# Optimization experiments

Hardware: AMD Instinct MI355X
Metric: run time of the kernel (lower is better)

Reference implementation:

```python
import jax, jax.numpy as jnp
import numpy as np

NUM_HEADS = 16
EMB = 1024
HEAD = 64
SEQ = 2048
BATCH = 4


def setup_inputs() -> dict:
    key = jax.random.key(0)
    ks = jax.random.split(key, 6)
    s = EMB ** -0.5
    x = jax.random.normal(ks[0], (BATCH, SEQ, EMB), dtype=jnp.float32)
    # per-head projection weights stacked: [H, E, D] (Linear(emb, head, bias=False) per head)
    Wq = jax.random.normal(ks[1], (NUM_HEADS, EMB, HEAD), dtype=jnp.float32) * s
    Wk = jax.random.normal(ks[2], (NUM_HEADS, EMB, HEAD), dtype=jnp.float32) * s
    Wv = jax.random.normal(ks[3], (NUM_HEADS, EMB, HEAD), dtype=jnp.float32) * s
    # output projection Linear(head*num_heads, emb): weight [E, H*D], bias [E]
    Wo = jax.random.normal(ks[4], (EMB, NUM_HEADS * HEAD), dtype=jnp.float32) * ((NUM_HEADS * HEAD) ** -0.5)
    bo = jax.random.normal(ks[5], (EMB,), dtype=jnp.float32) * 0.01
    return {"x": x, "Wq": Wq, "Wk": Wk, "Wv": Wv, "Wo": Wo, "bo": bo}


def reference(x, Wq, Wk, Wv, Wo, bo):
    B, S, E = x.shape
    scale = HEAD ** -0.5
    # batched per-head projections: [B, H, S, D]
    q = jnp.einsum('bse,hed->bhsd', x, Wq)
    k = jnp.einsum('bse,hed->bhsd', x, Wk)
    v = jnp.einsum('bse,hed->bhsd', x, Wv)
    scores = jnp.einsum('bhqd,bhkd->bhqk', q, k) * scale
    causal = jnp.tril(jnp.ones((S, S), dtype=bool))
    scores = jnp.where(causal, scores, jnp.finfo(scores.dtype).min)
    attn = jax.nn.softmax(scores, axis=-1)  # dropout disabled (eval/deterministic)
    ctx = jnp.einsum('bhqk,bhkd->bhqd', attn, v)
    # concat heads along last dim (head-major order, matching torch.cat)
    concat = ctx.transpose(0, 2, 1, 3).reshape(B, S, NUM_HEADS * HEAD)
    out = concat @ Wo.T + bo
    return out
```

## Files before the change

kernel.cpp:

```cpp
#include <hip/hip_runtime.h>

#define NHEADS 16
#define EMB 1024
#define HDIM 64
#define SEQ 2048
#define BATCH 4

typedef unsigned short u16;
typedef __attribute__((ext_vector_type(8))) __bf16 bf16x8;
typedef __attribute__((ext_vector_type(4))) float f32x4;

#if __has_builtin(__builtin_amdgcn_exp2f)
#define EXP2(x) __builtin_amdgcn_exp2f(x)
#else
#define EXP2(x) __expf((x)*0.69314718056f)
#endif
#define CL2E 0.18033688011112042f

#define BARRIER() __builtin_amdgcn_s_barrier()
#define SB0() __builtin_amdgcn_sched_barrier(0)
#define PRIO1() __builtin_amdgcn_s_setprio(1)
#define PRIO0() __builtin_amdgcn_s_setprio(0)
#define VMCNT(n) asm volatile("s_waitcnt vmcnt(" #n ")" ::: "memory")
#define LGKM0() asm volatile("s_waitcnt lgkmcnt(0)" ::: "memory")

__device__ __forceinline__ u16 f2bf(float f) {
  union { float f; unsigned u; } v; v.f = f;
  unsigned r = v.u + 0x7fffu + ((v.u >> 16) & 1u);
  return (u16)(r >> 16);
}
__device__ __forceinline__ unsigned pk2bf(float a, float b) {
  union { __bf16 h[2]; unsigned u; } x;
  x.h[0] = (__bf16)a; x.h[1] = (__bf16)b; return x.u;
}
__device__ __forceinline__ void gl16(const void* g, void* l) {
  __builtin_amdgcn_global_load_lds(
      (const __attribute__((address_space(1))) unsigned*)g,
      (__attribute__((address_space(3))) unsigned*)l, 16, 0, 0);
}
__device__ __forceinline__ unsigned PKLO(unsigned a, unsigned b) {
  return __builtin_amdgcn_perm(a, b, 0x01000504u);
}
__device__ __forceinline__ unsigned PKHI(unsigned a, unsigned b) {
  return __builtin_amdgcn_perm(a, b, 0x03020706u);
}

__global__ __launch_bounds__(256) void k_cvt(const float* __restrict__ in,
                                             u16* __restrict__ out, int n4) {
  int i = blockIdx.x * 256 + threadIdx.x;
  if (i >= n4) return;
  f32x4 v = *(const f32x4*)(in + (size_t)i * 4);
  uint2 o;
  o.x = (unsigned)f2bf(v[0]) | ((unsigned)f2bf(v[1]) << 16);
  o.y = (unsigned)f2bf(v[2]) | ((unsigned)f2bf(v[3]) << 16);
  *(uint2*)(out + (size_t)i * 4) = o;
}

__global__ __launch_bounds__(256) void k_packw(const float* __restrict__ Wq,
                                               const float* __restrict__ Wk,
                                               const float* __restrict__ Wv,
                                               u16* __restrict__ Wt) {
  const int mh = blockIdx.x;
  const int e0 = blockIdx.y * 64;
  const int mtx = mh >> 4, h = mh & 15;
  const float* W = (mtx == 0 ? Wq : (mtx == 1 ? Wk : Wv)) + (size_t)h * EMB * HDIM;
  __shared__ u16 sT[64][65];
  const int t = threadIdx.x;
  {
    int e = t >> 2, d0 = (t & 3) * 16;
#pragma unroll
    for (int jj = 0; jj < 4; jj++) {
      f32x4 v = *(const f32x4*)(W + (size_t)(e0 + e) * HDIM + d0 + jj * 4);
#pragma unroll
      for (int kk = 0; kk < 4; kk++) sT[e][d0 + jj * 4 + kk] = f2bf(v[kk]);
    }
  }
  __syncthreads();
  {
    int d = t >> 2, eb = (t & 3) * 16;
#pragma unroll
    for (int j = 0; j < 16; j++)
      Wt[(size_t)(mh * 64 + d) * EMB + e0 + eb + j] = sT[eb + j][d];
  }
}

__global__ __launch_bounds__(512, 2) void k_gemm_qkv8(const u16* __restrict__ Xb,
                                                      const u16* __restrict__ Wt,
                                                      u16* __restrict__ Q,
                                                      u16* __restrict__ K,
                                                      u16* __restrict__ V) {
  extern __shared__ __align__(16) char smem[];
  const int bid = blockIdx.x;
  const int l = (bid & 7) * 64 + (bid >> 3);
  const int mt = l & 31, nt = l >> 5;
  const int m0 = mt * 256, n0 = nt * 192;

  const int t = threadIdx.x;
  const int wave = t >> 6, lane = t & 63, lr = lane & 15, lg = lane >> 4;
  const int wr = (wave >> 2) * 128;
  const int wc = (wave & 3) * 48;

  const f32x4 fz = {0.f, 0.f, 0.f, 0.f};
  f32x4 acc[8][3];
#pragma unroll
  for (int i = 0; i < 8; i++)
#pragma unroll
    for (int j = 0; j < 3; j++) acc[i][j] = fz;

  bf16x8 af[4][2], bfr[3][2];

  auto SROUND = [&](char* ldsbase, int rbase, const u16* src, int gRowBase, int kt) {
    int rs = rbase + wave * 8;
    int row = rs + (lane >> 3);
    int gc = (lane & 7) ^ (row & 7);
    gl16(src + (size_t)(gRowBase + row) * EMB + kt * 64 + gc * 8, ldsbase + rs * 128);
  };
  auto LOADA = [&](const char* bA, int mh) {
#pragma unroll
    for (int mf = 0; mf < 4; mf++)
#pragma unroll
      for (int kf = 0; kf < 2; kf++) {
        int row = wr + mh * 64 + mf * 16 + lr;
        af[mf][kf] = *(const bf16x8*)(bA + row * 128 + ((kf * 64 + lg * 16) ^ ((row & 7) << 4)));
      }
  };
  auto LOADB = [&](const char* bB) {
#pragma unroll
    for (int nf = 0; nf < 3; nf++)
#pragma unroll
      for (int kf = 0; kf < 2; kf++) {
        int row = wc + nf * 16 + lr;
        bfr[nf][kf] = *(const bf16x8*)(bB + row * 128 + ((kf * 64 + lg * 16) ^ ((row & 7) << 4)));
      }
  };

#define MFMAPH(MH)                                                                         \
  do {                                                                                     \
    _Pragma("unroll") for (int kf = 0; kf < 2; kf++)                                       \
    _Pragma("unroll") for (int mf = 0; mf < 4; mf++)                                       \
    _Pragma("unroll") for (int nf = 0; nf < 3; nf++)                                       \
      acc[(MH)*4 + mf][nf] = __builtin_amdgcn_mfma_f32_16x16x32_bf16(                      \
          af[mf][kf], bfr[nf][kf], acc[(MH)*4 + mf][nf], 0, 0, 0);                         \
  } while (0)

  const int NT = EMB / 64;
  {
    char* nA = smem;
    char* nB = smem + 32768;
    SROUND(nB, 0, Wt, n0, 0); SROUND(nB, 64, Wt, n0, 0); SROUND(nB, 128, Wt, n0, 0);
    SROUND(nA, 0, Xb, m0, 0);
    SROUND(nA, 64, Xb, m0, 0); SROUND(nA, 128, Xb, m0, 0); SROUND(nA, 192, Xb, m0, 0);
  }
  VMCNT(0);
  BARRIER();

  for (int tt = 0; tt < NT - 1; tt++) {
    const int cb = tt & 1, nb = cb ^ 1;
    char* bA = smem + cb * 57344;
    char* bB = bA + 32768;
    char* nA = smem + nb * 57344;
    char* nB = nA + 32768;
    SROUND(nB, 0, Wt, n0, tt + 1);
    SROUND(nB, 64, Wt, n0, tt + 1);
    SROUND(nB, 128, Wt, n0, tt + 1);
    SROUND(nA, 0, Xb, m0, tt + 1);
    VMCNT(5);
    BARRIER(); SB0();
    LOADA(bA, 0);
    LOADB(bB);
    PRIO1(); MFMAPH(0); PRIO0();
    BARRIER();
    SROUND(nA, 64, Xb, m0, tt + 1);
    SROUND(nA, 128, Xb, m0, tt + 1);
    SROUND(nA, 192, Xb, m0, tt + 1);
    VMCNT(7);
    BARRIER(); SB0();
    LOADA(bA, 1);
    PRIO1(); MFMAPH(1); PRIO0();
    BARRIER();
  }
  {
    char* bA = smem + ((NT - 1) & 1) * 57344;
    char* bB = bA + 32768;
    VMCNT(0);
    BARRIER(); SB0();
    LOADA(bA, 0);
    LOADB(bB);
    PRIO1(); MFMAPH(0); PRIO0();
    LOADA(bA, 1);
    PRIO1(); MFMAPH(1); PRIO0();
  }
#undef MFMAPH

  const int b = m0 >> 11;
  const int s0 = m0 & 2047;
#pragma unroll
  for (int am = 0; am < 8; am++)
#pragma unroll
    for (int nf = 0; nf < 3; nf++)
#pragma unroll
      for (int r = 0; r < 4; r++) {
        int row = wr + am * 16 + lg * 4 + r;
        int n = n0 + wc + nf * 16 + lr;
        int mtx = n >> 10, h = (n >> 6) & 15, d = n & 63;
        u16* dst = (mtx == 0 ? Q : (mtx == 1 ? K : V));
        dst[((size_t)(b * NHEADS + h) * SEQ + s0 + row) * HDIM + d] = f2bf(acc[am][nf][r]);
      }
}

__global__ __launch_bounds__(256, 3) void k_attn(const u16* __restrict__ Q,
                                                 const u16* __restrict__ K,
                                                 const u16* __restrict__ V,
                                                 u16* __restrict__ Cc) {
  const int bh = blockIdx.x;
  const int qt = 15 - (int)blockIdx.y;
  const int b = bh >> 4, h = bh & 15;
  const int t = threadIdx.x;
  const int wq = t >> 6, lane = t & 63, lr = lane & 15, lg = lane >> 4;
  const size_t base = (size_t)bh * SEQ * HDIM;

  __shared__ __align__(16) char sK[2][64 * 128];
  __shared__ __align__(16) char sV[2][64 * 128];
  __shared__ __align__(16) char sP[128 * 128];

  const int kvb = (t & 15) * 4, db = (t >> 4) * 4;
  uint2 v0, v1, v2, v3;
  auto VLOAD = [&](int k0) {
    const u16* vp = V + base + (size_t)(k0 + kvb) * HDIM + db;
    v0 = *(const uint2*)(vp);
    v1 = *(const uint2*)(vp + HDIM);
    v2 = *(const uint2*)(vp + 2 * HDIM);
    v3 = *(const uint2*)(vp + 3 * HDIM);
  };
  auto VWRITE = [&](char* sv) {
    uint2 w0 = {PKLO(v0.x, v1.x), PKLO(v2.x, v3.x)};
    uint2 w1 = {PKHI(v0.x, v1.x), PKHI(v2.x, v3.x)};
    uint2 w2 = {PKLO(v0.y, v1.y), PKLO(v2.y, v3.y)};
    uint2 w3 = {PKHI(v0.y, v1.y), PKHI(v2.y, v3.y)};
    *(uint2*)(sv + (db + 0) * 128 + ((kvb * 2) ^ (((db + 0) & 7) << 4))) = w0;
    *(uint2*)(sv + (db + 1) * 128 + ((kvb * 2) ^ (((db + 1) & 7) << 4))) = w1;
    *(uint2*)(sv + (db + 2) * 128 + ((kvb * 2) ^ (((db + 2) & 7) << 4))) = w2;
    *(uint2*)(sv + (db + 3) * 128 + ((kvb * 2) ^ (((db + 3) & 7) << 4))) = w3;
  };
  auto KSTAGE = [&](char* sk, int k0) {
#pragma unroll
    for (int i = 0; i < 2; i++) {
      int rb = wq * 16 + i * 8;
      int row = rb + (lane >> 3);
      int gc = (lane & 7) ^ (row & 7);
      gl16(K + base + (size_t)(k0 + row) * HDIM + gc * 8, sk + rb * 128);
    }
  };

#pragma unroll
  for (int i = 0; i < 4; i++) {
    int rb = wq * 32 + i * 8;
    int row = rb + (lane >> 3);
    int gc = (lane & 7) ^ (row & 7);
    gl16(Q + base + (size_t)(qt * 128 + row) * HDIM + gc * 8, sP + rb * 128);
  }
  KSTAGE(sK[0], 0);
  VLOAD(0);
  VMCNT(0);
  VWRITE(sV[0]);
  __syncthreads();

  bf16x8 qf[2][2];
#pragma unroll
  for (int q2 = 0; q2 < 2; q2++)
#pragma unroll
    for (int kf = 0; kf < 2; kf++) {
      int row = wq * 32 + q2 * 16 + lr;
      qf[q2][kf] = *(const bf16x8*)(sP + row * 128 + ((kf * 64 + lg * 16) ^ ((row & 7) << 4)));
    }

  const f32x4 fz = {0.f, 0.f, 0.f, 0.f};
  f32x4 ot[4][2];
#pragma unroll
  for (int df = 0; df < 4; df++)
#pragma unroll
    for (int q2 = 0; q2 < 2; q2++) ot[df][q2] = fz;
  float m_[2] = {-1e30f, -1e30f}, l_[2] = {0.f, 0.f};

  const int nsteps = 2 * qt + 2;
  for (int step = 0; step < nsteps; step++) {
    const int k0 = step * 64;
    const int cur = step & 1, nxt = cur ^ 1;
    const bool pf = (step + 1 < nsteps);
    if (pf) {
      KSTAGE(sK[nxt], k0 + 64);
      VLOAD(k0 + 64);
    }

    f32x4 st[4][2];
#pragma unroll
    for (int kvf = 0; kvf < 4; kvf++)
#pragma unroll
      for (int q2 = 0; q2 < 2; q2++) st[kvf][q2] = fz;
#pragma unroll
    for (int kf = 0; kf < 2; kf++) {
      bf16x8 kfr[4];
#pragma unroll
      for (int kvf = 0; kvf < 4; kvf++) {
        int row = kvf * 16 + lr;
        kfr[kvf] = *(const bf16x8*)(sK[cur] + row * 128 + ((kf * 64 + lg * 16) ^ ((row & 7) << 4)));
      }
#pragma unroll
      for (int kvf = 0; kvf < 4; kvf++)
#pragma unroll
        for (int q2 = 0; q2 < 2; q2++)
          st[kvf][q2] = __builtin_amdgcn_mfma_f32_16x16x32_bf16(kfr[kvf], qf[q2][kf], st[kvf][q2], 0, 0, 0);
    }

    const bool diag = (k0 >= qt * 128);
    float mxv[2];
#pragma unroll
    for (int q2 = 0; q2 < 2; q2++) {
      if (diag) {
        const int qg = qt * 128 + wq * 32 + q2 * 16 + lr;
#pragma unroll
        for (int kvf = 0; kvf < 4; kvf++)
#pragma unroll
          for (int r = 0; r < 4; r++)
            if (k0 + kvf * 16 + 4 * lg + r > qg) st[kvf][q2][r] = -3e38f;
      }
      float mx = -3e38f;
#pragma unroll
      for (int kvf = 0; kvf < 4; kvf++)
        mx = fmaxf(mx, fmaxf(fmaxf(st[kvf][q2][0], st[kvf][q2][1]),
                             fmaxf(st[kvf][q2][2], st[kvf][q2][3])));
      mx = fmaxf(mx, __shfl_xor(mx, 16));
      mx = fmaxf(mx, __shfl_xor(mx, 32));
      mxv[q2] = mx;
    }
    if (!__all((mxv[0] <= m_[0] + 64.f) && (mxv[1] <= m_[1] + 64.f))) {
#pragma unroll
      for (int q2 = 0; q2 < 2; q2++) {
        float mnew = fmaxf(m_[q2], mxv[q2]);
        float alpha = EXP2((m_[q2] - mnew) * CL2E);
        m_[q2] = mnew;
        l_[q2] *= alpha;
#pragma unroll
        for (int df = 0; df < 4; df++) ot[df][q2] *= alpha;
      }
    }
#pragma unroll
    for (int q2 = 0; q2 < 2; q2++) {
      float nmc = -m_[q2] * CL2E;
      float rs = 0.f;
      const int prow = wq * 32 + q2 * 16 + lr;
#pragma unroll
      for (int kvf = 0; kvf < 4; kvf++) {
        float p0 = EXP2(fmaf(st[kvf][q2][0], CL2E, nmc));
        float p1 = EXP2(fmaf(st[kvf][q2][1], CL2E, nmc));
        float p2 = EXP2(fmaf(st[kvf][q2][2], CL2E, nmc));
        float p3 = EXP2(fmaf(st[kvf][q2][3], CL2E, nmc));
        rs += (p0 + p1) + (p2 + p3);
        uint2 w;
        w.x = pk2bf(p0, p1);
        w.y = pk2bf(p2, p3);
        *(uint2*)(sP + prow * 128 + ((kvf * 32 + lg * 8) ^ ((prow & 7) << 4))) = w;
      }
      rs += __shfl_xor(rs, 16);
      rs += __shfl_xor(rs, 32);
      l_[q2] += rs;
    }

#pragma unroll
    for (int kf = 0; kf < 2; kf++) {
      bf16x8 pfg[2], vf[4];
#pragma unroll
      for (int q2 = 0; q2 < 2; q2++) {
        int row = wq * 32 + q2 * 16 + lr;
        pfg[q2] = *(const bf16x8*)(sP + row * 128 + ((kf * 64 + lg * 16) ^ ((row & 7) << 4)));
      }
#pragma unroll
      for (int df = 0; df < 4; df++) {
        int row = df * 16 + lr;
        vf[df] = *(const bf16x8*)(sV[cur] + row * 128 + ((kf * 64 + lg * 16) ^ ((row & 7) << 4)));
      }
#pragma unroll
      for (int df = 0; df < 4; df++)
#pragma unroll
        for (int q2 = 0; q2 < 2; q2++)
          ot[df][q2] = __builtin_amdgcn_mfma_f32_16x16x32_bf16(vf[df], pfg[q2], ot[df][q2], 0, 0, 0);
    }

    if (pf) {
      VMCNT(0);
      VWRITE(sV[nxt]);
      LGKM0();
      BARRIER();
    }
  }

#pragma unroll
  for (int q2 = 0; q2 < 2; q2++) {
    float inv = 1.0f / l_[q2];
    int s = qt * 128 + wq * 32 + q2 * 16 + lr;
#pragma unroll
    for (int df = 0; df < 4; df++) {
      uint2 w;
      w.x = pk2bf(ot[df][q2][0] * inv, ot[df][q2][1] * inv);
      w.y = pk2bf(ot[df][q2][2] * inv, ot[df][q2][3] * inv);
      *(uint2*)(Cc + ((size_t)b * SEQ + s) * (NHEADS * HDIM) + h * HDIM + df * 16 + 4 * lg) = w;
    }
  }
}

__global__ __launch_bounds__(256) void k_gemm_out(const u16* __restrict__ Cc,
                                                  const u16* __restrict__ Wob,
                                                  const float* __restrict__ bo,
                                                  float* __restrict__ out) {
  const int m0 = blockIdx.x * 128;
  const int n0 = blockIdx.y * 128;
  const int t = threadIdx.x;
  const int wave = t >> 6, lane = t & 63, lr = lane & 15, lg = lane >> 4;
  const int wr = (wave >> 1) * 64, wc = (wave & 1) * 64;

  __shared__ __align__(16) char sA[128 * 128];
  __shared__ __align__(16) char sB[128 * 128];

  const f32x4 fz = {0.f, 0.f, 0.f, 0.f};
  f32x4 acc[4][4];
#pragma unroll
  for (int i = 0; i < 4; i++)
#pragma unroll
    for (int j = 0; j < 4; j++) acc[i][j] = fz;

  for (int k0 = 0; k0 < EMB; k0 += 64) {
#pragma unroll
    for (int i = 0; i < 4; i++) {
      int rb = wave * 32 + i * 8;
      int row = rb + (lane >> 3);
      int gc = (lane & 7) ^ (row & 7);
      gl16(Cc + (size_t)(m0 + row) * EMB + k0 + gc * 8, sA + rb * 128);
      gl16(Wob + (size_t)(n0 + row) * EMB + k0 + gc * 8, sB + rb * 128);
    }
    __syncthreads();
    bf16x8 af[4][2], bfr[4][2];
#pragma unroll
    for (int mf = 0; mf < 4; mf++)
#pragma unroll
      for (int kf = 0; kf < 2; kf++) {
        int row = wr + mf * 16 + lr;
        af[mf][kf] = *(const bf16x8*)(sA + row * 128 + ((kf * 64 + lg * 16) ^ ((row & 7) << 4)));
      }
#pragma unroll
    for (int nf = 0; nf < 4; nf++)
#pragma unroll
      for (int kf = 0; kf < 2; kf++) {
        int row = wc + nf * 16 + lr;
        bfr[nf][kf] = *(const bf16x8*)(sB + row * 128 + ((kf * 64 + lg * 16) ^ ((row & 7) << 4)));
      }
#pragma unroll
    for (int kf = 0; kf < 2; kf++)
#pragma unroll
      for (int mf = 0; mf < 4; mf++)
#pragma unroll
        for (int nf = 0; nf < 4; nf++)
          acc[mf][nf] = __builtin_amdgcn_mfma_f32_16x16x32_bf16(af[mf][kf], bfr[nf][kf], acc[mf][nf], 0, 0, 0);
    __syncthreads();
  }

  float bv[4];
#pragma unroll
  for (int nf = 0; nf < 4; nf++) bv[nf] = bo[n0 + wc + nf * 16 + lr];
#pragma unroll
  for (int mf = 0; mf < 4; mf++)
#pragma unroll
    for (int nf = 0; nf < 4; nf++)
#pragma unroll
      for (int r = 0; r < 4; r++) {
        int row = wr + mf * 16 + lg * 4 + r;
        int n = n0 + wc + nf * 16 + lr;
        out[(size_t)(m0 + row) * EMB + n] = acc[mf][nf][r] + bv[nf];
      }
}

extern "C" void kernel_launch(void* const* d_in, const int* in_sizes, int n_in,
                              void* d_out, int out_size, void* d_ws, size_t ws_size,
                              hipStream_t stream) {
  const float* x  = (const float*)d_in[0];
  const float* Wq = (const float*)d_in[1];
  const float* Wk = (const float*)d_in[2];
  const float* Wv = (const float*)d_in[3];
  const float* Wo = (const float*)d_in[4];
  const float* bo = (const float*)d_in[5];
  float* out = (float*)d_out;

  char* ws = (char*)d_ws;
  const size_t SZ_XB  = (size_t)8192 * 1024 * 2;
  const size_t SZ_WT  = (size_t)3072 * 1024 * 2;
  const size_t SZ_WOB = (size_t)1024 * 1024 * 2;
  const size_t SZ_QKV = (size_t)64 * 2048 * 64 * 2;
  u16* Xb  = (u16*)(ws);
  u16* Wt  = (u16*)(ws + SZ_XB);
  u16* Wob = (u16*)(ws + SZ_XB + SZ_WT);
  u16* Qb  = (u16*)(ws + SZ_XB + SZ_WT + SZ_WOB);
  u16* Kb  = (u16*)(ws + SZ_XB + SZ_WT + SZ_WOB + SZ_QKV);
  u16* Vb  = (u16*)(ws + SZ_XB + SZ_WT + SZ_WOB + 2 * SZ_QKV);
  u16* Cc  = (u16*)(ws + SZ_XB + SZ_WT + SZ_WOB + 3 * SZ_QKV);

  k_cvt<<<8192, 256, 0, stream>>>(x, Xb, 2097152);
  k_cvt<<<1024, 256, 0, stream>>>(Wo, Wob, 262144);
  k_packw<<<dim3(48, 16), 256, 0, stream>>>(Wq, Wk, Wv, Wt);
  k_gemm_qkv8<<<512, 512, 114688, stream>>>(Xb, Wt, Qb, Kb, Vb);
  k_attn<<<dim3(64, 16), 256, 0, stream>>>(Qb, Kb, Vb, Cc);
  k_gemm_out<<<dim3(64, 8), 256, 0, stream>>>(Cc, Wob, bo, out);
}
```

Baseline: 164.9 us.

## Rewrite output projection GEMM as 8-wave double-buffered pipelined kernel, add MFMA priority

Replaces the simple 128x128 output-projection GEMM, which synchronized twice per K step, with a 256x128-tile, 512-thread kernel. The new kernel double-buffers global-to-LDS loads across K tiles, splits each tile into two MFMA phases, uses a swizzled block order, and raises wave priority around MFMA clusters. It also adds s_setprio around the MFMA blocks in the attention kernel. The aim is to hide global load latency behind matrix work. The cost is more LDS use, fixed vmcnt accounting that is fragile, and fewer blocks in flight.

```diff
diff --git a/kernel.cpp b/kernel.cpp
--- a/kernel.cpp
+++ b/kernel.cpp
@@ -305,11 +305,13 @@
         int row = kvf * 16 + lr;
         kfr[kvf] = *(const bf16x8*)(sK[cur] + row * 128 + ((kf * 64 + lg * 16) ^ ((row & 7) << 4)));
       }
+      PRIO1();
 #pragma unroll
       for (int kvf = 0; kvf < 4; kvf++)
 #pragma unroll
         for (int q2 = 0; q2 < 2; q2++)
           st[kvf][q2] = __builtin_amdgcn_mfma_f32_16x16x32_bf16(kfr[kvf], qf[q2][kf], st[kvf][q2], 0, 0, 0);
+      PRIO0();
     }
 
     const bool diag = (k0 >= qt * 128);
@@ -379,11 +381,13 @@
         int row = df * 16 + lr;
         vf[df] = *(const bf16x8*)(sV[cur] + row * 128 + ((kf * 64 + lg * 16) ^ ((row & 7) << 4)));
       }
+      PRIO1();
 #pragma unroll
       for (int df = 0; df < 4; df++)
 #pragma unroll
         for (int q2 = 0; q2 < 2; q2++)
           ot[df][q2] = __builtin_amdgcn_mfma_f32_16x16x32_bf16(vf[df], pfg[q2], ot[df][q2], 0, 0, 0);
+      PRIO0();
     }
 
     if (pf) {
@@ -408,73 +412,124 @@
   }
 }
 
-__global__ __launch_bounds__(256) void k_gemm_out(const u16* __restrict__ Cc,
-                                                  const u16* __restrict__ Wob,
-                                                  const float* __restrict__ bo,
-                                                  float* __restrict__ out) {
-  const int m0 = blockIdx.x * 128;
-  const int n0 = blockIdx.y * 128;
+__global__ __launch_bounds__(512, 2) void k_gemm_out8(const u16* __restrict__ Cc,
+                                                      const u16* __restrict__ Wob,
+                                                      const float* __restrict__ bo,
+                                                      float* __restrict__ out) {
+  extern __shared__ __align__(16) char smem[];
+  const int bid = blockIdx.x;
+  const int l = (bid & 7) * 32 + (bid >> 3);
+  const int mt = l & 31, nt = l >> 5;
+  const int m0 = mt * 256, n0 = nt * 128;
+
   const int t = threadIdx.x;
   const int wave = t >> 6, lane = t & 63, lr = lane & 15, lg = lane >> 4;
-  const int wr = (wave >> 1) * 64, wc = (wave & 1) * 64;
-
-  __shared__ __align__(16) char sA[128 * 128];
-  __shared__ __align__(16) char sB[128 * 128];
+  const int wr = (wave >> 2) * 128;
+  const int wc = (wave & 3) * 32;
 
   const f32x4 fz = {0.f, 0.f, 0.f, 0.f};
-  f32x4 acc[4][4];
-#pragma unroll
-  for (int i = 0; i < 4; i++)
-#pragma unroll
-    for (int j = 0; j < 4; j++) acc[i][j] = fz;
-
-  for (int k0 = 0; k0 < EMB; k0 += 64) {
-#pragma unroll
-    for (int i = 0; i < 4; i++) {
-      int rb = wave * 32 + i * 8;
-      int row = rb + (lane >> 3);
-      int gc = (lane & 7) ^ (row & 7);
-      gl16(Cc + (size_t)(m0 + row) * EMB + k0 + gc * 8, sA + rb * 128);
-      gl16(Wob + (size_t)(n0 + row) * EMB + k0 + gc * 8, sB + rb * 128);
-    }
-    __syncthreads();
-    bf16x8 af[4][2], bfr[4][2];
+  f32x4 acc[8][2];
+#pragma unroll
+  for (int i = 0; i < 8; i++)
+#pragma unroll
+    for (int j = 0; j < 2; j++) acc[i][j] = fz;
+
+  bf16x8 af[4][2], bfr[2][2];
+
+  auto SROUND = [&](char* ldsbase, int rbase, const u16* src, int gRowBase, int kt) {
+    int rs = rbase + wave * 8;
+    int row = rs + (lane >> 3);
+    int gc = (lane & 7) ^ (row & 7);
+    gl16(src + (size_t)(gRowBase + row) * EMB + kt * 64 + gc * 8, ldsbase + rs * 128);
+  };
+  auto LOADA = [&](const char* bA, int mh) {
 #pragma unroll
     for (int mf = 0; mf < 4; mf++)
 #pragma unroll
       for (int kf = 0; kf < 2; kf++) {
-        int row = wr + mf * 16 + lr;
-        af[mf][kf] = *(const bf16x8*)(sA + row * 128 + ((kf * 64 + lg * 16) ^ ((row & 7) << 4)));
-      }
-#pragma unroll
-    for (int nf = 0; nf < 4; nf++)
+        int row = wr + mh * 64 + mf * 16 + lr;
+        af[mf][kf] = *(const bf16x8*)(bA + row * 128 + ((kf * 64 + lg * 16) ^ ((row & 7) << 4)));
+      }
+  };
+  auto LOADB = [&](const char* bB) {
+#pragma unroll
+    for (int nf = 0; nf < 2; nf++)
 #pragma unroll
       for (int kf = 0; kf < 2; kf++) {
         int row = wc + nf * 16 + lr;
-        bfr[nf][kf] = *(const bf16x8*)(sB + row * 128 + ((kf * 64 + lg * 16) ^ ((row & 7) << 4)));
-      }
-#pragma unroll
-    for (int kf = 0; kf < 2; kf++)
-#pragma unroll
-      for (int mf = 0; mf < 4; mf++)
-#pragma unroll
-        for (int nf = 0; nf < 4; nf++)
-          acc[mf][nf] = __builtin_amdgcn_mfma_f32_16x16x32_bf16(af[mf][kf], bfr[nf][kf], acc[mf][nf], 0, 0, 0);
-    __syncthreads();
-  }
-
-  float bv[4];
-#pragma unroll
-  for (int nf = 0; nf < 4; nf++) bv[nf] = bo[n0 + wc + nf * 16 + lr];
-#pragma unroll
-  for (int mf = 0; mf < 4; mf++)
-#pragma unroll
-    for (int nf = 0; nf < 4; nf++)
+        bfr[nf][kf] = *(const bf16x8*)(bB + row * 128 + ((kf * 64 + lg * 16) ^ ((row & 7) << 4)));
+      }
+  };
+
+#define MFMAPH2(MH)                                                                        \
+  do {                                                                                     \
+    _Pragma("unroll") for (int kf = 0; kf < 2; kf++)                                       \
+    _Pragma("unroll") for (int mf = 0; mf < 4; mf++)                                       \
+    _Pragma("unroll") for (int nf = 0; nf < 2; nf++)                                       \
+      acc[(MH)*4 + mf][nf] = __builtin_amdgcn_mfma_f32_16x16x32_bf16(                      \
+          af[mf][kf], bfr[nf][kf], acc[(MH)*4 + mf][nf], 0, 0, 0);                         \
+  } while (0)
+
+  const int NT = EMB / 64;
+  {
+    char* nA = smem;
+    char* nB = smem + 32768;
+    SROUND(nB, 0, Wob, n0, 0); SROUND(nB, 64, Wob, n0, 0);
+    SROUND(nA, 0, Cc, m0, 0);
+    SROUND(nA, 64, Cc, m0, 0); SROUND(nA, 128, Cc, m0, 0); SROUND(nA, 192, Cc, m0, 0);
+  }
+  VMCNT(0);
+  BARRIER();
+
+  for (int tt = 0; tt < NT - 1; tt++) {
+    const int cb = tt & 1, nb = cb ^ 1;
+    char* bA = smem + cb * 49152;
+    char* bB = bA + 32768;
+    char* nA = smem + nb * 49152;
+    char* nB = nA + 32768;
+    SROUND(nB, 0, Wob, n0, tt + 1);
+    SROUND(nB, 64, Wob, n0, tt + 1);
+    SROUND(nA, 0, Cc, m0, tt + 1);
+    VMCNT(4);
+    BARRIER(); SB0();
+    LOADA(bA, 0);
+    LOADB(bB);
+    PRIO1(); MFMAPH2(0); PRIO0();
+    BARRIER();
+    SROUND(nA, 64, Cc, m0, tt + 1);
+    SROUND(nA, 128, Cc, m0, tt + 1);
+    SROUND(nA, 192, Cc, m0, tt + 1);
+    VMCNT(6);
+    BARRIER(); SB0();
+    LOADA(bA, 1);
+    PRIO1(); MFMAPH2(1); PRIO0();
+    BARRIER();
+  }
+  {
+    char* bA = smem + ((NT - 1) & 1) * 49152;
+    char* bB = bA + 32768;
+    VMCNT(0);
+    BARRIER(); SB0();
+    LOADA(bA, 0);
+    LOADB(bB);
+    PRIO1(); MFMAPH2(0); PRIO0();
+    LOADA(bA, 1);
+    PRIO1(); MFMAPH2(1); PRIO0();
+  }
+#undef MFMAPH2
+
+  float bv[2];
+#pragma unroll
+  for (int nf = 0; nf < 2; nf++) bv[nf] = bo[n0 + wc + nf * 16 + lr];
+#pragma unroll
+  for (int am = 0; am < 8; am++)
+#pragma unroll
+    for (int nf = 0; nf < 2; nf++)
 #pragma unroll
       for (int r = 0; r < 4; r++) {
-        int row = wr + mf * 16 + lg * 4 + r;
+        int row = wr + am * 16 + lg * 4 + r;
         int n = n0 + wc + nf * 16 + lr;
-        out[(size_t)(m0 + row) * EMB + n] = acc[mf][nf][r] + bv[nf];
+        out[(size_t)(m0 + row) * EMB + n] = acc[am][nf][r] + bv[nf];
       }
 }
 
@@ -507,5 +562,5 @@
   k_packw<<<dim3(48, 16), 256, 0, stream>>>(Wq, Wk, Wv, Wt);
   k_gemm_qkv8<<<512, 512, 114688, stream>>>(Xb, Wt, Qb, Kb, Vb);
   k_attn<<<dim3(64, 16), 256, 0, stream>>>(Qb, Kb, Vb, Cc);
-  k_gemm_out<<<dim3(64, 8), 256, 0, stream>>>(Cc, Wob, bo, out);
-}
+  k_gemm_out8<<<256, 512, 98304, stream>>>(Cc, Wob, bo, out);
+}
```

Result: no change. 165.9 us (+0.6%).
